# Optimization experiments

Hardware: AMD Instinct MI355X
Metric: run time of the kernel (lower is better)

The kernel has to match this reference:

```python
import jax, jax.numpy as jnp
import numpy as np
from jax import lax

T, B, I, H, FC, O = 2048, 64, 128, 128, 32, 2

def _xavier(key, shape):
    # torch xavier_normal_ on [..., fan_out, fan_in]
    std = float(np.sqrt(2.0 / (shape[-2] + shape[-1])))
    return jax.random.normal(key, shape, jnp.float32) * std

def setup_inputs() -> dict:
    key = jax.random.key(0)
    ks = jax.random.split(key, 16)
    inp = {
        'x': jax.random.normal(ks[0], (T, B, I), jnp.float32),
        'w_ig': _xavier(ks[1], (B, H, I)),
        'w_ii': _xavier(ks[2], (B, H, I)),
        'w_if': _xavier(ks[3], (B, H, I)),
        'w_io': _xavier(ks[4], (B, H, I)),
        'w_hg': _xavier(ks[5], (B, H, H)),
        'w_hi': _xavier(ks[6], (B, H, H)),
        'w_hf': _xavier(ks[7], (B, H, H)),
        'w_ho': _xavier(ks[8], (B, H, H)),
        'b_g': jnp.zeros((B, H, 1), jnp.float32),
        'b_i': jnp.zeros((B, H, 1), jnp.float32),
        'b_f': jnp.zeros((B, H, 1), jnp.float32),
        'b_o': jnp.zeros((B, H, 1), jnp.float32),
        'fc1_w': _xavier(ks[9], (FC, H)),
        'fc1_b': jnp.zeros((FC,), jnp.float32),
        'fc2_w': _xavier(ks[10], (O, FC)),
        'fc2_b': jnp.zeros((O,), jnp.float32),
    }
    return inp

def reference(x, w_ig, w_ii, w_if, w_io, w_hg, w_hi, w_hf, w_ho,
              b_g, b_i, b_f, b_o, fc1_w, fc1_b, fc2_w, fc2_b):
    b, h = w_hg.shape[0], w_hg.shape[1]
    # Original bug: gates read self.hidd which is never updated -> stays zeros.
    hidd0 = jnp.zeros((b, h), x.dtype)
    # Recurrent contributions (identically zero, kept for faithfulness)
    rg = jnp.einsum('bhk,bk->bh', w_hg, hidd0)
    ri = jnp.einsum('bhk,bk->bh', w_hi, hidd0)
    rf = jnp.einsum('bhk,bk->bh', w_hf, hidd0)
    ro = jnp.einsum('bhk,bk->bh', w_ho, hidd0)
    # Input gate pre-activations for all timesteps in one einsum each: [T,B,H]
    g = jnp.tanh(jnp.einsum('bhi,tbi->tbh', w_ig, x) + rg + b_g[:, :, 0])
    i_ = jax.nn.sigmoid(jnp.einsum('bhi,tbi->tbh', w_ii, x) + ri + b_i[:, :, 0])
    f = jax.nn.sigmoid(jnp.einsum('bhi,tbi->tbh', w_if, x) + rf + b_f[:, :, 0])
    o = jax.nn.sigmoid(jnp.einsum('bhi,tbi->tbh', w_io, x) + ro + b_o[:, :, 0])

    def step(carry, gifo):
        c, _ = carry
        g_t, i_t, f_t, o_t = gifo
        c = f_t * c + i_t * g_t
        hid = o_t * jnp.tanh(c)
        return (c, hid), None

    c0 = jnp.zeros((b, h), x.dtype)
    (c_fin, h_fin), _ = lax.scan(step, (c0, c0), (g, i_, f, o))
    # classifier on last hidden: Linear -> tanh -> Linear -> log_softmax
    z = jnp.tanh(h_fin @ fc1_w.T + fc1_b) @ fc2_w.T + fc2_b
    return jax.nn.log_softmax(z, axis=1)
```

## Files before the change

### kernel.cpp

```cpp
#include <hip/hip_runtime.h>
#include <cstddef>

#define T_DIM 2048
#define B_DIM 64
#define I_DIM 128
#define H_DIM 128
#define FC_DIM 32
#define O_DIM 2

#define NC 16
#define TC (T_DIM / NC)
#define MT 8

typedef __attribute__((ext_vector_type(8))) short bf16x8;
typedef __attribute__((ext_vector_type(4))) float f32x4;

__device__ __forceinline__ short f2bf(float f) {
    union { float f; unsigned u; } v; v.f = f;
    unsigned r = (v.u + 0x7FFFu + ((v.u >> 16) & 1u)) >> 16;
    return (short)r;
}
__device__ __forceinline__ float bf2f(short s) {
    union { unsigned u; float f; } v;
    v.u = ((unsigned)(unsigned short)s) << 16;
    return v.f;
}
__device__ __forceinline__ float fast_sig(float x) {
    return __builtin_amdgcn_rcpf(1.0f + __expf(-x));
}
__device__ __forceinline__ float fast_tanh(float x) {
    return 2.0f * __builtin_amdgcn_rcpf(1.0f + __expf(-2.0f * x)) - 1.0f;
}

__global__ void convert_w_kernel(const float* __restrict__ wg,
                                 const float* __restrict__ wi,
                                 const float* __restrict__ wf,
                                 short* __restrict__ og,
                                 short* __restrict__ oi,
                                 short* __restrict__ of)
{
    const float* src = (blockIdx.y == 0) ? wg : (blockIdx.y == 1) ? wi : wf;
    short* dst       = (blockIdx.y == 0) ? og : (blockIdx.y == 1) ? oi : of;
    const size_t idx = ((size_t)blockIdx.x * 256 + threadIdx.x) * 8;
    float4 u0 = *(const float4*)(src + idx);
    float4 u1 = *(const float4*)(src + idx + 4);
    float a[8] = {u0.x, u0.y, u0.z, u0.w, u1.x, u1.y, u1.z, u1.w};
    bf16x8 hi;
#pragma unroll
    for (int j = 0; j < 8; ++j) hi[j] = f2bf(a[j]);
    *(bf16x8*)(dst + idx) = hi;
}

__global__ __launch_bounds__(512, 4)
void gates_scan_kernel(const float* __restrict__ x,
    const short* __restrict__ wg, const short* __restrict__ wi,
    const short* __restrict__ wf,
    const float* __restrict__ b_g, const float* __restrict__ b_i,
    const float* __restrict__ b_f,
    float* __restrict__ wsF, float* __restrict__ wsA)
{
    __shared__ short frag[MT * 2 * 4 * 64 * 8];

    const int L    = threadIdx.x & 63;
    const int wv   = threadIdx.x >> 6;
    const int col  = L & 15;
    const int quad = L >> 4;
    const int bid  = blockIdx.x;
    const int b     = bid & (B_DIM - 1);
    const int chunk = bid >> 6;

    const int h = wv * 16 + col;
    bf16x8 Bg[4], Bi[4], Bf[4];
    {
        const size_t wo = ((size_t)b * H_DIM + h) * I_DIM + quad * 8;
#pragma unroll
        for (int kk = 0; kk < 4; ++kk) {
            Bg[kk] = *(const bf16x8*)(wg + wo + kk * 32);
            Bi[kk] = *(const bf16x8*)(wi + wo + kk * 32);
            Bf[kk] = *(const bf16x8*)(wf + wo + kk * 32);
        }
    }
    const float biasg = b_g[b * H_DIM + h];
    const float biasi = b_i[b * H_DIM + h];
    const float biasf = b_f[b * H_DIM + h];

    {
        const int mt = wv;
        const int tl = (col >> 2) * 32 + mt * 4 + (col & 3);
        const float* xp = x + ((size_t)(chunk * TC + tl) * B_DIM + b) * I_DIM;
#pragma unroll
        for (int kk = 0; kk < 4; ++kk) {
            const int i0 = quad * 8 + kk * 32;
            float4 u0 = *(const float4*)(xp + i0);
            float4 u1 = *(const float4*)(xp + i0 + 4);
            float a[8] = {u0.x, u0.y, u0.z, u0.w, u1.x, u1.y, u1.z, u1.w};
            bf16x8 hi, lo;
#pragma unroll
            for (int j = 0; j < 8; ++j) {
                short hb = f2bf(a[j]);
                hi[j] = hb;
                lo[j] = f2bf(a[j] - bf2f(hb));
            }
            *(bf16x8*)(frag + ((((mt * 2 + 0) * 4 + kk) * 64) + L) * 8) = hi;
            *(bf16x8*)(frag + ((((mt * 2 + 1) * 4 + kk) * 64) + L) * 8) = lo;
        }
    }
    __syncthreads();

    float Fq = 1.0f, Aq = 0.0f;
#pragma unroll 2
    for (int mt = 0; mt < MT; ++mt) {
        bf16x8 ah[4], al[4];
#pragma unroll
        for (int kk = 0; kk < 4; ++kk) {
            ah[kk] = *(const bf16x8*)(frag + ((((mt * 2 + 0) * 4 + kk) * 64) + L) * 8);
            al[kk] = *(const bf16x8*)(frag + ((((mt * 2 + 1) * 4 + kk) * 64) + L) * 8);
        }
        f32x4 accg = {0.f, 0.f, 0.f, 0.f};
        f32x4 acci = {0.f, 0.f, 0.f, 0.f};
        f32x4 accf = {0.f, 0.f, 0.f, 0.f};
#pragma unroll
        for (int kk = 0; kk < 4; ++kk) {
            accg = __builtin_amdgcn_mfma_f32_16x16x32_bf16(ah[kk], Bg[kk], accg, 0, 0, 0);
            acci = __builtin_amdgcn_mfma_f32_16x16x32_bf16(ah[kk], Bi[kk], acci, 0, 0, 0);
            accf = __builtin_amdgcn_mfma_f32_16x16x32_bf16(ah[kk], Bf[kk], accf, 0, 0, 0);
            accg = __builtin_amdgcn_mfma_f32_16x16x32_bf16(al[kk], Bg[kk], accg, 0, 0, 0);
            acci = __builtin_amdgcn_mfma_f32_16x16x32_bf16(al[kk], Bi[kk], acci, 0, 0, 0);
            accf = __builtin_amdgcn_mfma_f32_16x16x32_bf16(al[kk], Bf[kk], accf, 0, 0, 0);
        }
#pragma unroll
        for (int r = 0; r < 4; ++r) {
            float g  = fast_tanh(accg[r] + biasg);
            float iv = fast_sig(acci[r] + biasi);
            float fv = fast_sig(accf[r] + biasf);
            Aq = fv * Aq + iv * g;
            Fq = fv * Fq;
        }
    }

    float Fo = __shfl_xor(Fq, 16, 64);
    float Ao = __shfl_xor(Aq, 16, 64);
    if ((quad & 1) == 0) { Aq = Fo * Aq + Ao; Fq = Fo * Fq; }
    else                 { Aq = Fq * Ao + Aq; Fq = Fq * Fo; }
    Fo = __shfl_xor(Fq, 32, 64);
    Ao = __shfl_xor(Aq, 32, 64);
    if (quad < 2) { Aq = Fo * Aq + Ao; Fq = Fo * Fq; }
    else          { Aq = Fq * Ao + Aq; Fq = Fq * Fo; }

    if (quad == 0) {
        const int idx = (b * NC + chunk) * H_DIM + h;
        wsF[idx] = Fq;
        wsA[idx] = Aq;
    }
}

__global__ void finish_kernel(const float* __restrict__ x,
    const float* __restrict__ w_io, const float* __restrict__ b_o,
    const float* __restrict__ fc1_w, const float* __restrict__ fc1_b,
    const float* __restrict__ fc2_w, const float* __restrict__ fc2_b,
    const float* __restrict__ wsF, const float* __restrict__ wsA,
    float* __restrict__ out)
{
    const int b = blockIdx.x;
    const int h = threadIdx.x;
    __shared__ float hf[H_DIM];
    __shared__ float z1[FC_DIM];

    float c = 0.0f;
#pragma unroll
    for (int nc = 0; nc < NC; ++nc) {
        const int idx = (b * NC + nc) * H_DIM + h;
        c = wsF[idx] * c + wsA[idx];
    }
    const float* xl = x + ((size_t)(T_DIM - 1) * B_DIM + b) * I_DIM;
    const float* wo = w_io + ((size_t)b * H_DIM + h) * I_DIM;
    float acc = b_o[b * H_DIM + h];
#pragma unroll 8
    for (int i = 0; i < I_DIM; i += 4) {
        float4 xa = *(const float4*)(xl + i);
        float4 wa = *(const float4*)(wo + i);
        acc += xa.x * wa.x + xa.y * wa.y + xa.z * wa.z + xa.w * wa.w;
    }
    const float o = 1.0f / (1.0f + expf(-acc));
    hf[h] = o * tanhf(c);
    __syncthreads();

    if (h < FC_DIM) {
        float a = fc1_b[h];
        const float* w1 = fc1_w + h * H_DIM;
        for (int i = 0; i < H_DIM; ++i) a += w1[i] * hf[i];
        z1[h] = tanhf(a);
    }
    __syncthreads();

    if (h == 0) {
        float z0 = fc2_b[0], zo1 = fc2_b[1];
        for (int j = 0; j < FC_DIM; ++j) {
            z0  += fc2_w[j] * z1[j];
            zo1 += fc2_w[FC_DIM + j] * z1[j];
        }
        const float m = fmaxf(z0, zo1);
        const float lse = m + logf(expf(z0 - m) + expf(zo1 - m));
        out[b * O_DIM + 0] = z0 - lse;
        out[b * O_DIM + 1] = zo1 - lse;
    }
}

extern "C" void kernel_launch(void* const* d_in, const int* in_sizes, int n_in,
                              void* d_out, int out_size, void* d_ws, size_t ws_size,
                              hipStream_t stream) {
    const float* x     = (const float*)d_in[0];
    const float* w_ig  = (const float*)d_in[1];
    const float* w_ii  = (const float*)d_in[2];
    const float* w_if  = (const float*)d_in[3];
    const float* w_io  = (const float*)d_in[4];
    const float* b_g   = (const float*)d_in[9];
    const float* b_i   = (const float*)d_in[10];
    const float* b_f   = (const float*)d_in[11];
    const float* b_o   = (const float*)d_in[12];
    const float* fc1_w = (const float*)d_in[13];
    const float* fc1_b = (const float*)d_in[14];
    const float* fc2_w = (const float*)d_in[15];
    const float* fc2_b = (const float*)d_in[16];

    const size_t NW = (size_t)B_DIM * H_DIM * I_DIM;
    short* wgc = (short*)d_ws;
    short* wic = wgc + NW;
    short* wfc = wic + NW;
    float* wsF = (float*)(wfc + NW);
    float* wsA = wsF + (size_t)B_DIM * NC * H_DIM;
    float* out = (float*)d_out;

    convert_w_kernel<<<dim3(NW / (256 * 8), 3), 256, 0, stream>>>(
        w_ig, w_ii, w_if, wgc, wic, wfc);

    gates_scan_kernel<<<dim3(B_DIM * NC), 512, 0, stream>>>(
        x, wgc, wic, wfc, b_g, b_i, b_f, wsF, wsA);

    finish_kernel<<<B_DIM, 128, 0, stream>>>(x, w_io, b_o, fc1_w, fc1_b,
                                             fc2_w, fc2_b, wsF, wsA, out);
}
```

Baseline: 165.4 us.

## Drop bf16 hi/lo split of x and fold log2e scaling into weights

```diff
diff --git a/kernel.cpp b/kernel.cpp
--- a/kernel.cpp
+++ b/kernel.cpp
@@ -1,4 +1,5 @@
 #include <hip/hip_runtime.h>
+#include <hip/hip_bf16.h>
 #include <cstddef>
 
 #define T_DIM 2048
@@ -12,24 +13,20 @@
 #define TC (T_DIM / NC)
 #define MT 8
 
+#define LOG2E  1.44269504088896f
+#define LOG2E2 2.88539008177793f
+
 typedef __attribute__((ext_vector_type(8))) short bf16x8;
 typedef __attribute__((ext_vector_type(4))) float f32x4;
 
-__device__ __forceinline__ short f2bf(float f) {
-    union { float f; unsigned u; } v; v.f = f;
-    unsigned r = (v.u + 0x7FFFu + ((v.u >> 16) & 1u)) >> 16;
-    return (short)r;
-}
-__device__ __forceinline__ float bf2f(short s) {
-    union { unsigned u; float f; } v;
-    v.u = ((unsigned)(unsigned short)s) << 16;
-    return v.f;
-}
-__device__ __forceinline__ float fast_sig(float x) {
-    return __builtin_amdgcn_rcpf(1.0f + __expf(-x));
-}
-__device__ __forceinline__ float fast_tanh(float x) {
-    return 2.0f * __builtin_amdgcn_rcpf(1.0f + __expf(-2.0f * x)) - 1.0f;
+__device__ __forceinline__ bf16x8 cvt8(const float* __restrict__ p) {
+    union { bf16x8 v; __hip_bfloat162 h2[4]; } u;
+#pragma unroll
+    for (int j = 0; j < 4; ++j) {
+        float2 f2 = {p[2 * j], p[2 * j + 1]};
+        u.h2[j] = __float22bfloat162_rn(f2);
+    }
+    return u.v;
 }
 
 __global__ void convert_w_kernel(const float* __restrict__ wg,
@@ -41,14 +38,13 @@
 {
     const float* src = (blockIdx.y == 0) ? wg : (blockIdx.y == 1) ? wi : wf;
     short* dst       = (blockIdx.y == 0) ? og : (blockIdx.y == 1) ? oi : of;
+    const float scale = (blockIdx.y == 0) ? LOG2E2 : LOG2E;
     const size_t idx = ((size_t)blockIdx.x * 256 + threadIdx.x) * 8;
     float4 u0 = *(const float4*)(src + idx);
     float4 u1 = *(const float4*)(src + idx + 4);
-    float a[8] = {u0.x, u0.y, u0.z, u0.w, u1.x, u1.y, u1.z, u1.w};
-    bf16x8 hi;
-#pragma unroll
-    for (int j = 0; j < 8; ++j) hi[j] = f2bf(a[j]);
-    *(bf16x8*)(dst + idx) = hi;
+    float a[8] = {u0.x * scale, u0.y * scale, u0.z * scale, u0.w * scale,
+                  u1.x * scale, u1.y * scale, u1.z * scale, u1.w * scale};
+    *(bf16x8*)(dst + idx) = cvt8(a);
 }
 
 __global__ __launch_bounds__(512, 4)
@@ -59,7 +55,7 @@
     const float* __restrict__ b_f,
     float* __restrict__ wsF, float* __restrict__ wsA)
 {
-    __shared__ short frag[MT * 2 * 4 * 64 * 8];
+    __shared__ short frag[MT * 4 * 64 * 8];
 
     const int L    = threadIdx.x & 63;
     const int wv   = threadIdx.x >> 6;
@@ -80,9 +76,9 @@
             Bf[kk] = *(const bf16x8*)(wf + wo + kk * 32);
         }
     }
-    const float biasg = b_g[b * H_DIM + h];
-    const float biasi = b_i[b * H_DIM + h];
-    const float biasf = b_f[b * H_DIM + h];
+    const float biasg = b_g[b * H_DIM + h] * LOG2E2;
+    const float biasi = b_i[b * H_DIM + h] * LOG2E;
+    const float biasf = b_f[b * H_DIM + h] * LOG2E;
 
     {
         const int mt = wv;
@@ -94,15 +90,7 @@
             float4 u0 = *(const float4*)(xp + i0);
             float4 u1 = *(const float4*)(xp + i0 + 4);
             float a[8] = {u0.x, u0.y, u0.z, u0.w, u1.x, u1.y, u1.z, u1.w};
-            bf16x8 hi, lo;
-#pragma unroll
-            for (int j = 0; j < 8; ++j) {
-                short hb = f2bf(a[j]);
-                hi[j] = hb;
-                lo[j] = f2bf(a[j] - bf2f(hb));
-            }
-            *(bf16x8*)(frag + ((((mt * 2 + 0) * 4 + kk) * 64) + L) * 8) = hi;
-            *(bf16x8*)(frag + ((((mt * 2 + 1) * 4 + kk) * 64) + L) * 8) = lo;
+            *(bf16x8*)(frag + (((mt * 4 + kk) * 64) + L) * 8) = cvt8(a);
         }
     }
     __syncthreads();
@@ -110,12 +98,10 @@
     float Fq = 1.0f, Aq = 0.0f;
 #pragma unroll 2
     for (int mt = 0; mt < MT; ++mt) {
-        bf16x8 ah[4], al[4];
-#pragma unroll
-        for (int kk = 0; kk < 4; ++kk) {
-            ah[kk] = *(const bf16x8*)(frag + ((((mt * 2 + 0) * 4 + kk) * 64) + L) * 8);
-            al[kk] = *(const bf16x8*)(frag + ((((mt * 2 + 1) * 4 + kk) * 64) + L) * 8);
-        }
+        bf16x8 ah[4];
+#pragma unroll
+        for (int kk = 0; kk < 4; ++kk)
+            ah[kk] = *(const bf16x8*)(frag + (((mt * 4 + kk) * 64) + L) * 8);
         f32x4 accg = {0.f, 0.f, 0.f, 0.f};
         f32x4 acci = {0.f, 0.f, 0.f, 0.f};
         f32x4 accf = {0.f, 0.f, 0.f, 0.f};
@@ -124,15 +110,15 @@
             accg = __builtin_amdgcn_mfma_f32_16x16x32_bf16(ah[kk], Bg[kk], accg, 0, 0, 0);
             acci = __builtin_amdgcn_mfma_f32_16x16x32_bf16(ah[kk], Bi[kk], acci, 0, 0, 0);
             accf = __builtin_amdgcn_mfma_f32_16x16x32_bf16(ah[kk], Bf[kk], accf, 0, 0, 0);
-            accg = __builtin_amdgcn_mfma_f32_16x16x32_bf16(al[kk], Bg[kk], accg, 0, 0, 0);
-            acci = __builtin_amdgcn_mfma_f32_16x16x32_bf16(al[kk], Bi[kk], acci, 0, 0, 0);
-            accf = __builtin_amdgcn_mfma_f32_16x16x32_bf16(al[kk], Bf[kk], accf, 0, 0, 0);
         }
 #pragma unroll
         for (int r = 0; r < 4; ++r) {
-            float g  = fast_tanh(accg[r] + biasg);
-            float iv = fast_sig(acci[r] + biasi);
-            float fv = fast_sig(accf[r] + biasf);
+            float g  = 2.0f * __builtin_amdgcn_rcpf(
+                           1.0f + __builtin_amdgcn_exp2f(-(accg[r] + biasg))) - 1.0f;
+            float iv = __builtin_amdgcn_rcpf(
+                           1.0f + __builtin_amdgcn_exp2f(-(acci[r] + biasi)));
+            float fv = __builtin_amdgcn_rcpf(
+                           1.0f + __builtin_amdgcn_exp2f(-(accf[r] + biasf)));
             Aq = fv * Aq + iv * g;
             Fq = fv * Fq;
         }
```

Result: faster. 156.3 us (-5.5%).
